# Kernel tuning notes

Hardware: AMD Instinct MI355X
Metric: run time of the kernel (lower is better)

Reference implementation:

```python
import jax, jax.numpy as jnp
import numpy as np

T, E, H = 65536, 512, 512  # seq_len, embedding_size, hidden_size (kernel_size=2)


def setup_inputs() -> dict:
    key = jax.random.key(0)
    k1, k2 = jax.random.split(key)
    x = jax.random.normal(k1, (T, E), dtype=jnp.float32)
    # nn.Linear(2*E, 3*H): weight [3H, 2E], bias [3H]. Store transposed for x @ W.
    W = jax.random.normal(k2, (2 * E, 3 * H), dtype=jnp.float32) * 0.02
    b = jnp.zeros((3 * H,), dtype=jnp.float32)
    return {"input": x, "W": W, "b": b}


def reference(input, W, b):
    x = input
    t, e = x.shape
    h_dim = W.shape[1] // 3
    # Shift input by one step (zero-padded) and concat: conv over kernel_size=2 window.
    x_prev = jnp.concatenate([jnp.zeros((1, e), x.dtype), x[:-1]], axis=0)  # [T, E]
    gates = jnp.concatenate([x, x_prev], axis=1) @ W + b  # [T, 3H]
    z = jnp.tanh(gates[:, :h_dim])                # cell candidate
    f = jax.nn.sigmoid(gates[:, h_dim:2 * h_dim])  # forget gate
    o = jax.nn.sigmoid(gates[:, 2 * h_dim:])       # output gate

    # fo-pool recurrence: c_t = f_t * c_{t-1} + (1 - f_t) * z_t ; h_t = o_t * c_t
    def step(c, zfo):
        z_t, f_t, o_t = zfo
        c_new = f_t * c + (1.0 - f_t) * z_t
        return c_new, (c_new, o_t * c_new)

    c0 = jnp.zeros((h_dim,), x.dtype)
    _, (cells, hiddens) = jax.lax.scan(step, c0, (z, f, o))
    # Match torch: (hidden_temp [T,H], h [1,H], c [1,H])
    return hiddens, hiddens[-1:], cells[-1:]
```

## Files before the change

### kernel.cpp

```cpp
#include <hip/hip_runtime.h>


#define T_LEN 65536
#define E_DIM 512
#define H3    1536
#define K_DIM 1024
#define LC    256
#define NCHUNK (T_LEN / LC)

typedef float f32x4 __attribute__((ext_vector_type(4)));
typedef short bf16x8 __attribute__((ext_vector_type(8)));

__device__ __forceinline__ unsigned short f2bf(float f) {
    unsigned int x = __builtin_bit_cast(unsigned int, f);
    x += 0x7fffu + ((x >> 16) & 1u);
    return (unsigned short)(x >> 16);
}
__device__ __forceinline__ float bf2f(unsigned short u) {
    return __builtin_bit_cast(float, ((unsigned int)u) << 16);
}
__device__ __forceinline__ float fsig(float x)  { return 1.f / (1.f + __expf(-x)); }
__device__ __forceinline__ float ftanh(float x) { return 2.f / (1.f + __expf(-2.f * x)) - 1.f; }

__device__ __forceinline__ void gload_lds16(const void* g, void* l) {
    __builtin_amdgcn_global_load_lds((const __attribute__((address_space(1))) void*)g,
                                     (__attribute__((address_space(3))) void*)l, 16, 0, 0);
}

__global__ void prep_x(const float* __restrict__ x, unsigned short* __restrict__ xp) {
    const long long nq = (512LL + (long long)T_LEN * E_DIM) / 4;
    for (long long q = (long long)blockIdx.x * blockDim.x + threadIdx.x; q < nq;
         q += (long long)gridDim.x * blockDim.x) {
        ushort4 u;
        if (q < 128) {
            u.x = 0; u.y = 0; u.z = 0; u.w = 0;
        } else {
            const float4 v = *reinterpret_cast<const float4*>(x + q * 4 - 512);
            u.x = f2bf(v.x); u.y = f2bf(v.y); u.z = f2bf(v.z); u.w = f2bf(v.w);
        }
        *reinterpret_cast<ushort4*>(xp + q * 4) = u;
    }
}

__global__ void prep_w(const float* __restrict__ W, unsigned short* __restrict__ Wt) {
    const int n_el = K_DIM * H3;
    for (int i = blockIdx.x * blockDim.x + threadIdx.x; i < n_el;
         i += gridDim.x * blockDim.x) {
        const int k = i / H3, n = i - k * H3;
        Wt[n * K_DIM + k] = f2bf(W[i]);
    }
}

__global__ __launch_bounds__(256) void gemm_gates(
    const unsigned short* __restrict__ xp,
    const unsigned short* __restrict__ Wt,
    const float* __restrict__ bias,
    unsigned short* __restrict__ zfo)
{
    __shared__ unsigned short Alds[128 * 32];
    __shared__ unsigned short Blds[128 * 32];

    const int tid  = threadIdx.x;
    const int lane = tid & 63;
    const int w    = tid >> 6;
    const int wr   = w >> 1, wc = w & 1;

    const int  nt = blockIdx.x;
    const int  mt = blockIdx.y;
    const long long t0 = (long long)mt * 128;
    const int  nb = nt * 128;

    f32x4 acc[4][4] = {};

    const int r_in = lane >> 2;
    const int c8   = (lane & 3) * 8;
    const int ko   = (lane >> 4) * 8;
    const int l15  = lane & 15;

    for (int kt = 0; kt < 32; ++kt) {
        const int kb = kt * 32;
        const long long abase = (kb >= 512) ? (long long)(kb - 512) : (long long)(512 + kb);
        __syncthreads();
        #pragma unroll
        for (int j = 0; j < 2; ++j) {
            const int row = j * 64 + w * 16 + r_in;
            const unsigned short* ga = xp + abase + (t0 + row) * 512 + c8;
            gload_lds16(ga, &Alds[(j * 64 + w * 16) * 32]);
            const unsigned short* gb = Wt + (long long)(nb + row) * 1024 + kb + c8;
            gload_lds16(gb, &Blds[(j * 64 + w * 16) * 32]);
        }
        __syncthreads();
        bf16x8 af[4], bfr[4];
        #pragma unroll
        for (int m = 0; m < 4; ++m)
            af[m] = *reinterpret_cast<const bf16x8*>(&Alds[(wr * 64 + m * 16 + l15) * 32 + ko]);
        #pragma unroll
        for (int n = 0; n < 4; ++n)
            bfr[n] = *reinterpret_cast<const bf16x8*>(&Blds[(wc * 64 + n * 16 + l15) * 32 + ko]);
        #pragma unroll
        for (int m = 0; m < 4; ++m)
            #pragma unroll
            for (int n = 0; n < 4; ++n)
                acc[m][n] = __builtin_amdgcn_mfma_f32_16x16x32_bf16(af[m], bfr[n], acc[m][n], 0, 0, 0);
    }

    const int cls = nb >> 9;
    float bn[4];
    #pragma unroll
    for (int n = 0; n < 4; ++n) bn[n] = bias[nb + wc * 64 + n * 16 + l15];
    #pragma unroll
    for (int m = 0; m < 4; ++m) {
        #pragma unroll
        for (int n = 0; n < 4; ++n) {
            const int col = nb + wc * 64 + n * 16 + l15;
            #pragma unroll
            for (int j = 0; j < 4; ++j) {
                const long long row = t0 + wr * 64 + m * 16 + (lane >> 4) * 4 + j;
                float v = acc[m][n][j] + bn[n];
                v = (cls == 0) ? ftanh(v) : fsig(v);
                zfo[row * H3 + col] = f2bf(v);
            }
        }
    }
}

__global__ void scan_pass1(const unsigned short* __restrict__ zfo,
                           float* __restrict__ P, float* __restrict__ L) {
    const int chunk = blockIdx.x >> 1;
    const int ch    = (blockIdx.x & 1) * 256 + threadIdx.x;
    const long long tbase = (long long)chunk * LC;
    float c = 0.f, p = 1.f;
    #pragma unroll 4
    for (int t = 0; t < LC; ++t) {
        const long long off = (tbase + t) * H3;
        const float z = bf2f(zfo[off + ch]);
        const float f = bf2f(zfo[off + 512 + ch]);
        c = f * c + (1.f - f) * z;
        p *= f;
    }
    P[chunk * 512 + ch] = p;
    L[chunk * 512 + ch] = c;
}

__global__ void scan_pass2(const float* __restrict__ P, const float* __restrict__ L,
                           float* __restrict__ carry, float* __restrict__ out) {
    const int ch = threadIdx.x;
    float c = 0.f;
    for (int k = 0; k < NCHUNK; ++k) {
        carry[k * 512 + ch] = c;
        c = P[k * 512 + ch] * c + L[k * 512 + ch];
    }
    out[(long long)T_LEN * 512 + 512 + ch] = c;
}

__global__ void scan_pass3(const unsigned short* __restrict__ zfo,
                           const float* __restrict__ carry,
                           float* __restrict__ out) {
    const int chunk = blockIdx.x >> 1;
    const int ch    = (blockIdx.x & 1) * 256 + threadIdx.x;
    float c = carry[chunk * 512 + ch];
    const long long tbase = (long long)chunk * LC;
    float h = 0.f;
    #pragma unroll 4
    for (int t = 0; t < LC; ++t) {
        const long long off = (tbase + t) * H3;
        const float z = bf2f(zfo[off + ch]);
        const float f = bf2f(zfo[off + 512 + ch]);
        const float o = bf2f(zfo[off + 1024 + ch]);
        c = f * c + (1.f - f) * z;
        h = o * c;
        out[(tbase + t) * 512 + ch] = h;
    }
    if (chunk == NCHUNK - 1) out[(long long)T_LEN * 512 + ch] = h;
}

extern "C" void kernel_launch(void* const* d_in, const int* in_sizes, int n_in,
                              void* d_out, int out_size, void* d_ws, size_t ws_size,
                              hipStream_t stream) {
    const float* x = (const float*)d_in[0];
    const float* W = (const float*)d_in[1];
    const float* b = (const float*)d_in[2];
    float* out = (float*)d_out;

    char* ws = (char*)d_ws;
    unsigned short* xp  = (unsigned short*)(ws);
    unsigned short* Wt  = (unsigned short*)(ws + 67110912LL);
    unsigned short* zfo = (unsigned short*)(ws + 70256640LL);
    float* P     = (float*)(ws + 271583232LL);
    float* L     = (float*)(ws + 272107520LL);
    float* carry = (float*)(ws + 272631808LL);

    prep_x<<<4096, 256, 0, stream>>>(x, xp);
    prep_w<<<768, 256, 0, stream>>>(W, Wt);

    dim3 gg(H3 / 128, T_LEN / 128, 1);
    gemm_gates<<<gg, 256, 0, stream>>>(xp, Wt, b, zfo);

    scan_pass1<<<NCHUNK * 2, 256, 0, stream>>>(zfo, P, L);
    scan_pass2<<<1, 512, 0, stream>>>(P, L, carry, out);
    scan_pass3<<<NCHUNK * 2, 256, 0, stream>>>(zfo, carry, out);
}
```

Baseline: 461.9 us.

## Rewrite GEMM as 256x256 double-buffered pipeline and parallelize chunk scan

The gate GEMM moves to 256x256 tiles with 512 threads, a 64-wide K step, XOR-swizzled LDS, double-buffered async global-to-LDS loads interleaved with MFMA quarters, and s_setprio. The chunked scan uses smaller chunks (64 steps) with 4-channel vectorized loads and float4 stores. The serial carry pass becomes a parallel Hillis-Steele scan per channel in LDS. P/L/carry buffers now alias the xp workspace region, which is dead by then. The aim is more data reuse in the GEMM, overlap of memory with compute, and removal of the serial 256-step carry loop, at the cost of heavier register pressure and intricate manual barriers.

Measured after the change: 520.8 us. +12.7%, slower.

```diff
diff --git a/kernel.cpp b/kernel.cpp
--- a/kernel.cpp
+++ b/kernel.cpp
@@ -2,11 +2,10 @@
 
 
 #define T_LEN 65536
-#define E_DIM 512
 #define H3    1536
-#define K_DIM 1024
-#define LC    256
-#define NCHUNK (T_LEN / LC)
+#define NT    16
+#define LC    64
+#define NCHUNK 1024
 
 typedef float f32x4 __attribute__((ext_vector_type(4)));
 typedef short bf16x8 __attribute__((ext_vector_type(8)));
@@ -27,8 +26,12 @@
                                      (__attribute__((address_space(3))) void*)l, 16, 0, 0);
 }
 
+#define SB()    __builtin_amdgcn_sched_barrier(0)
+#define BARX()  __builtin_amdgcn_s_barrier()
+#define LGKM0() asm volatile("s_waitcnt lgkmcnt(0)" ::: "memory")
+
 __global__ void prep_x(const float* __restrict__ x, unsigned short* __restrict__ xp) {
-    const long long nq = (512LL + (long long)T_LEN * E_DIM) / 4;
+    const long long nq = (512LL + (long long)T_LEN * 512) / 4;
     for (long long q = (long long)blockIdx.x * blockDim.x + threadIdx.x; q < nq;
          q += (long long)gridDim.x * blockDim.x) {
         ushort4 u;
@@ -43,82 +46,152 @@
 }
 
 __global__ void prep_w(const float* __restrict__ W, unsigned short* __restrict__ Wt) {
-    const int n_el = K_DIM * H3;
+    const int n_el = 1024 * H3;
     for (int i = blockIdx.x * blockDim.x + threadIdx.x; i < n_el;
          i += gridDim.x * blockDim.x) {
         const int k = i / H3, n = i - k * H3;
-        Wt[n * K_DIM + k] = f2bf(W[i]);
-    }
-}
-
-__global__ __launch_bounds__(256) void gemm_gates(
+        Wt[n * 1024 + k] = f2bf(W[i]);
+    }
+}
+
+#define RD_A(m, ks) (*(const bf16x8*)(ldsAr + bo + ((m)*16 + arow)*64 + ((ks) ? colel1 : colel0)))
+#define RD_B(n, ks) (*(const bf16x8*)(ldsBr + bo + ((n)*16 + arow)*64 + ((ks) ? colel1 : colel0)))
+
+#define QUAD(mh, nh)                                                                     \
+    _Pragma("unroll")                                                                    \
+    for (int mm = 0; mm < 4; ++mm) {                                                     \
+        _Pragma("unroll")                                                                \
+        for (int nn = 0; nn < 2; ++nn) {                                                 \
+            acc[(mh)*4+mm][(nh)*2+nn] = __builtin_amdgcn_mfma_f32_16x16x32_bf16(         \
+                a[(mh)*4+mm][0], b[(nh)*2+nn][0], acc[(mh)*4+mm][(nh)*2+nn], 0, 0, 0);   \
+            acc[(mh)*4+mm][(nh)*2+nn] = __builtin_amdgcn_mfma_f32_16x16x32_bf16(         \
+                a[(mh)*4+mm][1], b[(nh)*2+nn][1], acc[(mh)*4+mm][(nh)*2+nn], 0, 0, 0);   \
+        }                                                                                \
+    }
+
+__global__ __launch_bounds__(512, 2) void gemm_gates(
     const unsigned short* __restrict__ xp,
     const unsigned short* __restrict__ Wt,
     const float* __restrict__ bias,
     unsigned short* __restrict__ zfo)
 {
-    __shared__ unsigned short Alds[128 * 32];
-    __shared__ unsigned short Blds[128 * 32];
+    __shared__ unsigned short lds[2 * 4 * 8192];
 
     const int tid  = threadIdx.x;
     const int lane = tid & 63;
-    const int w    = tid >> 6;
-    const int wr   = w >> 1, wc = w & 1;
-
-    const int  nt = blockIdx.x;
-    const int  mt = blockIdx.y;
-    const long long t0 = (long long)mt * 128;
-    const int  nb = nt * 128;
-
-    f32x4 acc[4][4] = {};
-
-    const int r_in = lane >> 2;
-    const int c8   = (lane & 3) * 8;
-    const int ko   = (lane >> 4) * 8;
-    const int l15  = lane & 15;
-
-    for (int kt = 0; kt < 32; ++kt) {
-        const int kb = kt * 32;
-        const long long abase = (kb >= 512) ? (long long)(kb - 512) : (long long)(512 + kb);
-        __syncthreads();
+    const int wid  = tid >> 6;
+    const int wm   = wid >> 2;
+    const int wn   = wid & 3;
+
+    const int bn0 = blockIdx.x * 256;
+    const int bm0 = blockIdx.y * 256;
+
+    const int srow = tid >> 3;
+    const int scol = (((tid & 7) ^ ((tid >> 3) & 7)) * 8);
+    const int aoff = (bm0 + srow) * 512 + scol;
+    const int boff = (bn0 + srow) * 1024 + scol;
+    unsigned short* ldsw = (unsigned short*)lds + wid * 512;
+
+    auto stageA = [&](int bb, int s, int kb) {
+        const int abase = (kb < 512) ? (512 + kb) : (kb - 512);
+        const unsigned short* g = xp + abase + aoff + s * (128 * 512);
+        unsigned short* l = ldsw + (bb * 4 + s) * 8192;
+        gload_lds16(g, l);
+        gload_lds16(g + 64 * 512, l + 4096);
+    };
+    auto stageB = [&](int bb, int s, int kb) {
+        const unsigned short* g = Wt + boff + kb + s * (128 * 1024);
+        unsigned short* l = ldsw + (bb * 4 + 2 + s) * 8192;
+        gload_lds16(g, l);
+        gload_lds16(g + 64 * 1024, l + 4096);
+    };
+
+    const int arow   = lane & 15;
+    const int colel0 = (((lane >> 4) * 16)      ^ ((lane & 7) << 4)) >> 1;
+    const int colel1 = ((64 + (lane >> 4) * 16) ^ ((lane & 7) << 4)) >> 1;
+    const unsigned short* ldsAr = (const unsigned short*)lds + wm * 8192;
+    const unsigned short* ldsBr = (const unsigned short*)lds + (2 + (wn >> 1)) * 8192 + (wn & 1) * 4096;
+
+    f32x4  acc[8][4] = {};
+    bf16x8 a[8][2]   = {};
+    bf16x8 b[4][2]   = {};
+
+    stageA(0, 0, 0);  stageA(0, 1, 0);  stageB(0, 0, 0);  stageB(0, 1, 0);
+    stageA(1, 0, 64); stageA(1, 1, 64); stageB(1, 0, 64);
+    asm volatile("s_waitcnt vmcnt(6)" ::: "memory");
+    SB(); BARX(); SB();
+
+    for (int t = 0; t < NT; ++t) {
+        const int buf = t & 1;
+        const int bo  = buf * 32768;
+
+        {
+            #pragma unroll
+            for (int m = 0; m < 4; ++m) { a[m][0] = RD_A(m, 0); a[m][1] = RD_A(m, 1); }
+            if (wm == 0) {
+                #pragma unroll
+                for (int m = 4; m < 8; ++m) { a[m][0] = RD_A(m, 0); a[m][1] = RD_A(m, 1); }
+            }
+            #pragma unroll
+            for (int n = 0; n < 2; ++n) { b[n][0] = RD_B(n, 0); b[n][1] = RD_B(n, 1); }
+            if (t + 1 < NT) stageB(buf ^ 1, 1, (t + 1) * 64);
+            SB(); BARX(); SB();
+            LGKM0(); SB();
+            __builtin_amdgcn_s_setprio(1);
+            QUAD(0, 0);
+            __builtin_amdgcn_s_setprio(0);
+            SB(); BARX(); SB();
+        }
+        {
+            if (wm == 1) {
+                #pragma unroll
+                for (int m = 4; m < 8; ++m) { a[m][0] = RD_A(m, 0); a[m][1] = RD_A(m, 1); }
+            }
+            #pragma unroll
+            for (int n = 2; n < 4; ++n) { b[n][0] = RD_B(n, 0); b[n][1] = RD_B(n, 1); }
+            if (t + 2 < NT) stageA(buf, 0, (t + 2) * 64);
+            SB(); BARX(); SB();
+            LGKM0(); SB();
+            __builtin_amdgcn_s_setprio(1);
+            QUAD(0, 1);
+            __builtin_amdgcn_s_setprio(0);
+            SB(); BARX(); SB();
+        }
+        {
+            if (t + 2 < NT) stageA(buf, 1, (t + 2) * 64);
+            SB(); BARX(); SB();
+            __builtin_amdgcn_s_setprio(1);
+            QUAD(1, 0);
+            __builtin_amdgcn_s_setprio(0);
+            SB(); BARX(); SB();
+        }
+        {
+            if (t + 2 < NT) stageB(buf, 0, (t + 2) * 64);
+            SB(); BARX(); SB();
+            __builtin_amdgcn_s_setprio(1);
+            QUAD(1, 1);
+            __builtin_amdgcn_s_setprio(0);
+            if (t < NT - 2)       { asm volatile("s_waitcnt vmcnt(6)" ::: "memory"); }
+            else if (t == NT - 2) { asm volatile("s_waitcnt vmcnt(0)" ::: "memory"); }
+            SB(); BARX(); SB();
+        }
+    }
+
+    const int cls   = bn0 >> 9;
+    const int r0    = bm0 + wm * 128 + ((lane >> 4) << 2);
+    const int cbase = bn0 + wn * 64 + (lane & 15);
+    #pragma unroll
+    for (int n = 0; n < 4; ++n) {
+        const int col = cbase + n * 16;
+        const float bn_ = bias[col];
         #pragma unroll
-        for (int j = 0; j < 2; ++j) {
-            const int row = j * 64 + w * 16 + r_in;
-            const unsigned short* ga = xp + abase + (t0 + row) * 512 + c8;
-            gload_lds16(ga, &Alds[(j * 64 + w * 16) * 32]);
-            const unsigned short* gb = Wt + (long long)(nb + row) * 1024 + kb + c8;
-            gload_lds16(gb, &Blds[(j * 64 + w * 16) * 32]);
-        }
-        __syncthreads();
-        bf16x8 af[4], bfr[4];
-        #pragma unroll
-        for (int m = 0; m < 4; ++m)
-            af[m] = *reinterpret_cast<const bf16x8*>(&Alds[(wr * 64 + m * 16 + l15) * 32 + ko]);
-        #pragma unroll
-        for (int n = 0; n < 4; ++n)
-            bfr[n] = *reinterpret_cast<const bf16x8*>(&Blds[(wc * 64 + n * 16 + l15) * 32 + ko]);
-        #pragma unroll
-        for (int m = 0; m < 4; ++m)
-            #pragma unroll
-            for (int n = 0; n < 4; ++n)
-                acc[m][n] = __builtin_amdgcn_mfma_f32_16x16x32_bf16(af[m], bfr[n], acc[m][n], 0, 0, 0);
-    }
-
-    const int cls = nb >> 9;
-    float bn[4];
-    #pragma unroll
-    for (int n = 0; n < 4; ++n) bn[n] = bias[nb + wc * 64 + n * 16 + l15];
-    #pragma unroll
-    for (int m = 0; m < 4; ++m) {
-        #pragma unroll
-        for (int n = 0; n < 4; ++n) {
-            const int col = nb + wc * 64 + n * 16 + l15;
+        for (int m = 0; m < 8; ++m) {
+            const int row = r0 + m * 16;
             #pragma unroll
             for (int j = 0; j < 4; ++j) {
-                const long long row = t0 + wr * 64 + m * 16 + (lane >> 4) * 4 + j;
-                float v = acc[m][n][j] + bn[n];
+                float v = acc[m][n][j] + bn_;
                 v = (cls == 0) ? ftanh(v) : fsig(v);
-                zfo[row * H3 + col] = f2bf(v);
+                zfo[(row + j) * H3 + col] = f2bf(v);
             }
         }
     }
@@ -126,52 +199,84 @@
 
 __global__ void scan_pass1(const unsigned short* __restrict__ zfo,
                            float* __restrict__ P, float* __restrict__ L) {
-    const int chunk = blockIdx.x >> 1;
-    const int ch    = (blockIdx.x & 1) * 256 + threadIdx.x;
-    const long long tbase = (long long)chunk * LC;
-    float c = 0.f, p = 1.f;
-    #pragma unroll 4
+    const int chunk = blockIdx.x;
+    const int c4    = threadIdx.x;
+    const unsigned short* base = zfo + (long long)chunk * LC * H3 + c4 * 4;
+    float c[4] = {0.f, 0.f, 0.f, 0.f};
+    float p[4] = {1.f, 1.f, 1.f, 1.f};
     for (int t = 0; t < LC; ++t) {
-        const long long off = (tbase + t) * H3;
-        const float z = bf2f(zfo[off + ch]);
-        const float f = bf2f(zfo[off + 512 + ch]);
-        c = f * c + (1.f - f) * z;
-        p *= f;
-    }
-    P[chunk * 512 + ch] = p;
-    L[chunk * 512 + ch] = c;
-}
-
-__global__ void scan_pass2(const float* __restrict__ P, const float* __restrict__ L,
-                           float* __restrict__ carry, float* __restrict__ out) {
-    const int ch = threadIdx.x;
-    float c = 0.f;
-    for (int k = 0; k < NCHUNK; ++k) {
-        carry[k * 512 + ch] = c;
-        c = P[k * 512 + ch] * c + L[k * 512 + ch];
-    }
-    out[(long long)T_LEN * 512 + 512 + ch] = c;
+        const unsigned short* row = base + t * H3;
+        const ushort4 uz = *reinterpret_cast<const ushort4*>(row);
+        const ushort4 uf = *reinterpret_cast<const ushort4*>(row + 512);
+        const float z[4] = {bf2f(uz.x), bf2f(uz.y), bf2f(uz.z), bf2f(uz.w)};
+        const float f[4] = {bf2f(uf.x), bf2f(uf.y), bf2f(uf.z), bf2f(uf.w)};
+        #pragma unroll
+        for (int j = 0; j < 4; ++j) {
+            c[j] = fmaf(f[j], c[j] - z[j], z[j]);
+            p[j] *= f[j];
+        }
+    }
+    #pragma unroll
+    for (int j = 0; j < 4; ++j) {
+        P[chunk * 512 + c4 * 4 + j] = p[j];
+        L[chunk * 512 + c4 * 4 + j] = c[j];
+    }
+}
+
+__global__ __launch_bounds__(1024) void scan_pass2(
+    const float* __restrict__ P, const float* __restrict__ L,
+    float* __restrict__ carry, float* __restrict__ out) {
+    const int ch = blockIdx.x;
+    const int k  = threadIdx.x;
+    __shared__ float sP[1024], sL[1024];
+    float p = P[k * 512 + ch];
+    float l = L[k * 512 + ch];
+    sP[k] = p; sL[k] = l;
+    __syncthreads();
+    for (int d = 1; d < 1024; d <<= 1) {
+        float pp = 1.f, ll = 0.f;
+        if (k >= d) { pp = sP[k - d]; ll = sL[k - d]; }
+        __syncthreads();
+        l = fmaf(p, ll, l);
+        p = p * pp;
+        sP[k] = p; sL[k] = l;
+        __syncthreads();
+    }
+    carry[k * 512 + ch] = (k == 0) ? 0.f : sL[k - 1];
+    if (k == 1023) out[(long long)T_LEN * 512 + 512 + ch] = l;
 }
 
 __global__ void scan_pass3(const unsigned short* __restrict__ zfo,
                            const float* __restrict__ carry,
                            float* __restrict__ out) {
-    const int chunk = blockIdx.x >> 1;
-    const int ch    = (blockIdx.x & 1) * 256 + threadIdx.x;
-    float c = carry[chunk * 512 + ch];
-    const long long tbase = (long long)chunk * LC;
-    float h = 0.f;
-    #pragma unroll 4
+    const int chunk = blockIdx.x;
+    const int c4    = threadIdx.x;
+    const unsigned short* base = zfo + (long long)chunk * LC * H3 + c4 * 4;
+    float c[4], h[4] = {0.f, 0.f, 0.f, 0.f};
+    #pragma unroll
+    for (int j = 0; j < 4; ++j) c[j] = carry[chunk * 512 + c4 * 4 + j];
+    float4* outp = reinterpret_cast<float4*>(out + (long long)chunk * LC * 512) + c4;
     for (int t = 0; t < LC; ++t) {
-        const long long off = (tbase + t) * H3;
-        const float z = bf2f(zfo[off + ch]);
-        const float f = bf2f(zfo[off + 512 + ch]);
-        const float o = bf2f(zfo[off + 1024 + ch]);
-        c = f * c + (1.f - f) * z;
-        h = o * c;
-        out[(tbase + t) * 512 + ch] = h;
-    }
-    if (chunk == NCHUNK - 1) out[(long long)T_LEN * 512 + ch] = h;
+        const unsigned short* row = base + t * H3;
+        const ushort4 uz = *reinterpret_cast<const ushort4*>(row);
+        const ushort4 uf = *reinterpret_cast<const ushort4*>(row + 512);
+        const ushort4 uo = *reinterpret_cast<const ushort4*>(row + 1024);
+        const float z[4] = {bf2f(uz.x), bf2f(uz.y), bf2f(uz.z), bf2f(uz.w)};
+        const float f[4] = {bf2f(uf.x), bf2f(uf.y), bf2f(uf.z), bf2f(uf.w)};
+        const float o[4] = {bf2f(uo.x), bf2f(uo.y), bf2f(uo.z), bf2f(uo.w)};
+        #pragma unroll
+        for (int j = 0; j < 4; ++j) {
+            c[j] = fmaf(f[j], c[j] - z[j], z[j]);
+            h[j] = o[j] * c[j];
+        }
+        float4 hv; hv.x = h[0]; hv.y = h[1]; hv.z = h[2]; hv.w = h[3];
+        outp[t * 128] = hv;
+    }
+    if (chunk == NCHUNK - 1) {
+        #pragma unroll
+        for (int j = 0; j < 4; ++j)
+            out[(long long)T_LEN * 512 + c4 * 4 + j] = h[j];
+    }
 }
 
 extern "C" void kernel_launch(void* const* d_in, const int* in_sizes, int n_in,
@@ -186,17 +291,17 @@
     unsigned short* xp  = (unsigned short*)(ws);
     unsigned short* Wt  = (unsigned short*)(ws + 67110912LL);
     unsigned short* zfo = (unsigned short*)(ws + 70256640LL);
-    float* P     = (float*)(ws + 271583232LL);
-    float* L     = (float*)(ws + 272107520LL);
-    float* carry = (float*)(ws + 272631808LL);
+    float* P     = (float*)(ws);
+    float* L     = (float*)(ws + 4194304LL);
+    float* carry = (float*)(ws + 8388608LL);
 
     prep_x<<<4096, 256, 0, stream>>>(x, xp);
     prep_w<<<768, 256, 0, stream>>>(W, Wt);
 
-    dim3 gg(H3 / 128, T_LEN / 128, 1);
-    gemm_gates<<<gg, 256, 0, stream>>>(xp, Wt, b, zfo);
-
-    scan_pass1<<<NCHUNK * 2, 256, 0, stream>>>(zfo, P, L);
-    scan_pass2<<<1, 512, 0, stream>>>(P, L, carry, out);
-    scan_pass3<<<NCHUNK * 2, 256, 0, stream>>>(zfo, carry, out);
-}
+    dim3 gg(H3 / 256, T_LEN / 256, 1);
+    gemm_gates<<<gg, 512, 0, stream>>>(xp, Wt, b, zfo);
+
+    scan_pass1<<<NCHUNK, 128, 0, stream>>>(zfo, P, L);
+    scan_pass2<<<512, 1024, 0, stream>>>(P, L, carry, out);
+    scan_pass3<<<NCHUNK, 128, 0, stream>>>(zfo, carry, out);
+}
```
